# Kernel optimization log

Measured on AMD Instinct MI355X. Metric: run time of the kernel, lower is better.

Reference implementation:

```python
import jax, jax.numpy as jnp
import numpy as np

N_NODES = 50000
N_EDGES = 800000
E_DIM = 128
N_LAYERS = 3
IN_DIM = 2
OUT_DIM = 1


def _lin_init(key, fan_in, fan_out, scale=None):
    # rough kaiming-tanh init, exact values don't matter for correctness testing
    s = scale if scale is not None else (5.0 / 3.0) / np.sqrt(fan_in)
    return jax.random.normal(key, (fan_in, fan_out), dtype=jnp.float32) * s


def setup_inputs() -> dict:
    key = jax.random.key(0)
    ks = jax.random.split(key, 16)
    node_feature = jax.random.normal(ks[0], (N_NODES, IN_DIM), dtype=jnp.float32)
    edge_index = jax.random.randint(ks[1], (2, N_EDGES), 0, N_NODES)
    batch = jnp.zeros((N_NODES,), dtype=jnp.int32)

    enc_W = _lin_init(ks[2], IN_DIM, E_DIM)
    enc_b = jnp.zeros((E_DIM,), dtype=jnp.float32)

    def stack(k, fan_in, fan_out):
        kk = jax.random.split(k, N_LAYERS)
        return jnp.stack([_lin_init(kk[i], fan_in, fan_out) for i in range(N_LAYERS)])

    gate_W = stack(ks[3], E_DIM, E_DIM)
    gate_b = jnp.zeros((N_LAYERS, E_DIM), dtype=jnp.float32)
    att_W = stack(ks[4], E_DIM, E_DIM)
    att_b = jnp.zeros((N_LAYERS, E_DIM), dtype=jnp.float32)
    msg_W = stack(ks[5], E_DIM, E_DIM)
    msg_b = jnp.zeros((N_LAYERS, E_DIM), dtype=jnp.float32)
    upd_W = stack(ks[6], 2 * E_DIM, E_DIM)
    upd_b = jnp.zeros((N_LAYERS, E_DIM), dtype=jnp.float32)

    dec1_W = _lin_init(ks[7], E_DIM, E_DIM // 2)
    dec1_b = jnp.zeros((E_DIM // 2,), dtype=jnp.float32)
    dec2_W = _lin_init(ks[8], E_DIM // 2, OUT_DIM, scale=1.0 / np.sqrt(E_DIM // 2))
    dec2_b = jnp.zeros((OUT_DIM,), dtype=jnp.float32)

    return dict(node_feature=node_feature, edge_index=edge_index, batch=batch,
                enc_W=enc_W, enc_b=enc_b,
                gate_W=gate_W, gate_b=gate_b, att_W=att_W, att_b=att_b,
                msg_W=msg_W, msg_b=msg_b, upd_W=upd_W, upd_b=upd_b,
                dec1_W=dec1_W, dec1_b=dec1_b, dec2_W=dec2_W, dec2_b=dec2_b)


def _segment_softmax(x, seg, num_segments):
    # PyG softmax over segments, numerically stable, per-channel
    m = jax.ops.segment_max(x, seg, num_segments=num_segments)
    m = jnp.where(jnp.isfinite(m), m, 0.0)
    e = jnp.exp(x - m[seg])
    s = jax.ops.segment_sum(e, seg, num_segments=num_segments)
    return e / (s[seg] + 1e-16)


def reference(node_feature, edge_index, batch,
              enc_W, enc_b, gate_W, gate_b, att_W, att_b,
              msg_W, msg_b, upd_W, upd_b,
              dec1_W, dec1_b, dec2_W, dec2_b):
    n = node_feature.shape[0]
    src, dst = edge_index[0], edge_index[1]  # j -> i (source_to_target)
    h = jnp.tanh(node_feature @ enc_W + enc_b)  # [N, E_DIM]
    for l in range(N_LAYERS):
        mj = jnp.tanh(h[src] @ msg_W[l] + msg_b[l])          # messages [Edges, E_DIM]
        gate = mj @ gate_W[l] + gate_b[l]                     # gate_nn (Linear only)
        alpha = _segment_softmax(gate, dst, n)                # softmax over incoming edges
        v = jnp.tanh(mj @ att_W[l] + att_b[l])                # attention_mlp
        aggr = jax.ops.segment_sum(alpha * v, dst, num_segments=n)
        h = jnp.tanh(jnp.concatenate([h, aggr], axis=1) @ upd_W[l] + upd_b[l])
    out = jnp.tanh(h @ dec1_W + dec1_b)
    out = out @ dec2_W + dec2_b
    return out
```

## Files before the change

### kernel.cpp

```cpp
#include <hip/hip_runtime.h>
#include <math.h>

#define ED 128
#define PROW 256

typedef _Float16 f16;
typedef _Float16 half8 __attribute__((ext_vector_type(8)));
typedef _Float16 half4 __attribute__((ext_vector_type(4)));
typedef float f32x4 __attribute__((ext_vector_type(4)));

static __device__ __forceinline__ float tanh_fast(float x) {
  float ax = fabsf(x);
  float e = __expf(2.0f * ax);
  float t = 1.0f - 2.0f / (e + 1.0f);
  return __builtin_copysignf(t, x);
}

static __device__ __forceinline__ void stage_w(
    const char* __restrict__ gsrc, int rowBytes, int rowOff,
    char* lds, int tid, int nIter) {
  #pragma unroll
  for (int i = 0; i < nIter; ++i) {
    int b = (i * 256 + tid) * 16;
    int row = b >> 8;
    int sw = (b & 255) ^ ((row & 7) << 4);
    float4 v = *reinterpret_cast<const float4*>(
        gsrc + (size_t)row * rowBytes + rowOff + sw);
    *reinterpret_cast<float4*>(lds + b) = v;
  }
}

static __device__ __forceinline__ half8 read_w(const char* Wsb, int col, int koff) {
  int byte = col * 256 + (koff ^ ((col & 7) << 4));
  return *reinterpret_cast<const half8*>(Wsb + byte);
}

__global__ __launch_bounds__(256) void encoder_kernel(
    const float* __restrict__ x, const float* __restrict__ W,
    const float* __restrict__ b, f16* __restrict__ h, int n) {
  int idx = blockIdx.x * blockDim.x + threadIdx.x;
  if (idx >= n * ED) return;
  int i = idx >> 7, c = idx & 127;
  float v = x[i * 2 + 0] * W[c] + x[i * 2 + 1] * W[ED + c] + b[c];
  h[idx] = (f16)tanh_fast(v);
}

__global__ __launch_bounds__(256) void transpose_w_kernel(
    const float* __restrict__ src, f16* __restrict__ dst, int K, int C, int total) {
  int idx = blockIdx.x * 256 + threadIdx.x;
  if (idx >= total) return;
  int kc = K * C;
  int m = idx / kc;
  int rem = idx - m * kc;
  int c = rem / K;
  int k = rem - c * K;
  dst[idx] = (f16)src[(size_t)m * kc + (size_t)k * C + c];
}

__global__ __launch_bounds__(256) void transpose3_kernel(
    const float* __restrict__ s0, const float* __restrict__ s1,
    const float* __restrict__ s2, f16* __restrict__ d0,
    f16* __restrict__ d1, f16* __restrict__ d2) {
  int idx = blockIdx.x * 256 + threadIdx.x;
  const int per = 3 * 128 * 128;
  int which = idx / per;
  if (which >= 3) return;
  int rem = idx - which * per;
  const float* s = (which == 0) ? s0 : (which == 1) ? s1 : s2;
  f16* d = (which == 0) ? d0 : (which == 1) ? d1 : d2;
  int m = rem >> 14;
  int r2 = rem & 16383;
  int c = r2 >> 7, k = r2 & 127;
  d[rem] = (f16)s[m * 16384 + k * 128 + c];
}

__global__ __launch_bounds__(256) void count_deg_kernel(
    const int* __restrict__ dst, int* __restrict__ deg, int E) {
  int e = blockIdx.x * blockDim.x + threadIdx.x;
  if (e < E) atomicAdd(&deg[dst[e]], 1);
}

__global__ __launch_bounds__(1024) void scan_kernel(
    const int* __restrict__ deg, int* __restrict__ offs,
    int* __restrict__ cursor, int n) {
  __shared__ int wsum[16];
  __shared__ int carry_s;
  const int tid = threadIdx.x;
  const int lane = tid & 63;
  const int wid = tid >> 6;
  if (tid == 0) carry_s = 0;
  __syncthreads();
  for (int base = 0; base < n; base += 1024) {
    const int i = base + tid;
    const int v = (i < n) ? deg[i] : 0;
    int x = v;
    #pragma unroll
    for (int d = 1; d < 64; d <<= 1) {
      int t = __shfl_up(x, d, 64);
      if (lane >= d) x += t;
    }
    if (lane == 63) wsum[wid] = x;
    __syncthreads();
    int wbase = 0, total = 0;
    #pragma unroll
    for (int w = 0; w < 16; ++w) {
      int s = wsum[w];
      if (w < wid) wbase += s;
      total += s;
    }
    const int carry = carry_s;
    if (i < n) {
      const int excl = carry + wbase + x - v;
      offs[i] = excl;
      cursor[i] = excl;
    }
    __syncthreads();
    if (tid == 0) carry_s = carry + total;
    __syncthreads();
  }
  if (tid == 0) offs[n] = carry_s;
}

__global__ __launch_bounds__(256) void scatter_kernel(
    const int* __restrict__ src, const int* __restrict__ dst,
    int* __restrict__ cursor, int* __restrict__ ssrc, int E) {
  int e = blockIdx.x * blockDim.x + threadIdx.x;
  if (e < E) {
    int d = dst[e];
    int pos = atomicAdd(&cursor[d], 1);
    ssrc[pos] = src[e];
  }
}


__global__ __launch_bounds__(256) void gemm_mgv_kernel(
    const f16* __restrict__ h,
    const f16* __restrict__ mWt, const float* __restrict__ mb,
    const f16* __restrict__ gWt, const float* __restrict__ gb,
    const f16* __restrict__ aWt, const float* __restrict__ ab,
    f16* __restrict__ P, int n) {
  __shared__ f16 Ws[128 * 128];
  __shared__ f16 Ss[64 * 128];
  char* Wsb = reinterpret_cast<char*>(Ws);
  char* Sb = reinterpret_cast<char*>(Ss);
  const int tid = threadIdx.x;
  const int w = tid >> 6, lane = tid & 63;
  const int lr = lane & 15, lg = lane >> 4;
  const int r0 = blockIdx.x * 64 + w * 16;

  half8 a[4];
  {
    int rr = r0 + lr;
    if (rr >= n) rr = n - 1;
    const f16* ap = h + (size_t)rr * ED + lg * 8;
    #pragma unroll
    for (int kt = 0; kt < 4; ++kt)
      a[kt] = *reinterpret_cast<const half8*>(ap + kt * 32);
  }

  stage_w((const char*)mWt, 256, 0, Wsb, tid, 8);
  __syncthreads();
  #pragma unroll
  for (int t = 0; t < 8; ++t) {
    f32x4 acc = {0.f, 0.f, 0.f, 0.f};
    int col = t * 16 + lr;
    #pragma unroll
    for (int kt = 0; kt < 4; ++kt)
      acc = __builtin_amdgcn_mfma_f32_16x16x32_f16(a[kt], read_w(Wsb, col, lg * 16 + kt * 64), acc, 0, 0, 0);
    float bias = mb[col];
    #pragma unroll
    for (int j = 0; j < 4; ++j) {
      int srow = w * 16 + lg * 4 + j;
      int byte = srow * 256 + (((col * 2) ^ ((srow & 7) << 4)));
      *reinterpret_cast<f16*>(Sb + byte) = (f16)tanh_fast(acc[j] + bias);
    }
  }
  half8 ma[4];
  {
    int lrow = w * 16 + lr;
    #pragma unroll
    for (int kt = 0; kt < 4; ++kt) {
      int byte = lrow * 256 + ((lg * 16 + kt * 64) ^ ((lrow & 7) << 4));
      ma[kt] = *reinterpret_cast<const half8*>(Sb + byte);
    }
  }
  __syncthreads();

  stage_w((const char*)gWt, 256, 0, Wsb, tid, 8);
  __syncthreads();
  float wreg[8][4];
  #pragma unroll
  for (int t = 0; t < 8; ++t) {
    f32x4 acc = {0.f, 0.f, 0.f, 0.f};
    int col = t * 16 + lr;
    #pragma unroll
    for (int kt = 0; kt < 4; ++kt)
      acc = __builtin_amdgcn_mfma_f32_16x16x32_f16(ma[kt], read_w(Wsb, col, lg * 16 + kt * 64), acc, 0, 0, 0);
    float bias = gb[col];
    #pragma unroll
    for (int j = 0; j < 4; ++j) {
      float ww = fminf(__expf(acc[j] + bias), 60000.f);
      wreg[t][j] = ww;
      int grow = r0 + lg * 4 + j;
      if (grow < n) P[(size_t)grow * PROW + col] = (f16)ww;
    }
  }
  __syncthreads();

  stage_w((const char*)aWt, 256, 0, Wsb, tid, 8);
  __syncthreads();
  #pragma unroll
  for (int t = 0; t < 8; ++t) {
    f32x4 acc = {0.f, 0.f, 0.f, 0.f};
    int col = t * 16 + lr;
    #pragma unroll
    for (int kt = 0; kt < 4; ++kt)
      acc = __builtin_amdgcn_mfma_f32_16x16x32_f16(ma[kt], read_w(Wsb, col, lg * 16 + kt * 64), acc, 0, 0, 0);
    float bias = ab[col];
    #pragma unroll
    for (int j = 0; j < 4; ++j) {
      int grow = r0 + lg * 4 + j;
      if (grow < n)
        P[(size_t)grow * PROW + 128 + col] = (f16)(wreg[t][j] * tanh_fast(acc[j] + bias));
    }
  }
}

__global__ __launch_bounds__(256) void updmgv_kernel(
    const f16* __restrict__ h, const f16* __restrict__ ag,
    const f16* __restrict__ uWt, const float* __restrict__ ub,
    const f16* __restrict__ mWt, const float* __restrict__ mb,
    const f16* __restrict__ gWt, const float* __restrict__ gb,
    const f16* __restrict__ aWt, const float* __restrict__ ab,
    f16* __restrict__ hout, f16* __restrict__ P, int n) {
  __shared__ f16 Ws[128 * 128];
  __shared__ f16 Ss[64 * 128];
  char* Wsb = reinterpret_cast<char*>(Ws);
  char* Sb = reinterpret_cast<char*>(Ss);
  const int tid = threadIdx.x;
  const int w = tid >> 6, lane = tid & 63;
  const int lr = lane & 15, lg = lane >> 4;
  const int r0 = blockIdx.x * 64 + w * 16;

  half8 ah[4], aa[4];
  {
    int rr = r0 + lr;
    if (rr >= n) rr = n - 1;
    const f16* ap = h + (size_t)rr * ED + lg * 8;
    const f16* bp = ag + (size_t)rr * ED + lg * 8;
    #pragma unroll
    for (int kt = 0; kt < 4; ++kt) {
      ah[kt] = *reinterpret_cast<const half8*>(ap + kt * 32);
      aa[kt] = *reinterpret_cast<const half8*>(bp + kt * 32);
    }
  }

  stage_w((const char*)uWt, 512, 0, Wsb, tid, 8);
  __syncthreads();
  f32x4 acc8[8];
  #pragma unroll
  for (int t = 0; t < 8; ++t) {
    f32x4 acc = {0.f, 0.f, 0.f, 0.f};
    int col = t * 16 + lr;
    #pragma unroll
    for (int kt = 0; kt < 4; ++kt)
      acc = __builtin_amdgcn_mfma_f32_16x16x32_f16(ah[kt], read_w(Wsb, col, lg * 16 + kt * 64), acc, 0, 0, 0);
    acc8[t] = acc;
  }
  __syncthreads();
  stage_w((const char*)uWt, 512, 256, Wsb, tid, 8);
  __syncthreads();
  #pragma unroll
  for (int t = 0; t < 8; ++t) {
    f32x4 acc = acc8[t];
    int col = t * 16 + lr;
    #pragma unroll
    for (int kt = 0; kt < 4; ++kt)
      acc = __builtin_amdgcn_mfma_f32_16x16x32_f16(aa[kt], read_w(Wsb, col, lg * 16 + kt * 64), acc, 0, 0, 0);
    float bias = ub[col];
    #pragma unroll
    for (int j = 0; j < 4; ++j) {
      f16 hv = (f16)tanh_fast(acc[j] + bias);
      int srow = w * 16 + lg * 4 + j;
      int byte = srow * 256 + (((col * 2) ^ ((srow & 7) << 4)));
      *reinterpret_cast<f16*>(Sb + byte) = hv;
      int grow = r0 + lg * 4 + j;
      if (grow < n) hout[(size_t)grow * ED + col] = hv;
    }
  }
  half8 ha[4];
  {
    int lrow = w * 16 + lr;
    #pragma unroll
    for (int kt = 0; kt < 4; ++kt) {
      int byte = lrow * 256 + ((lg * 16 + kt * 64) ^ ((lrow & 7) << 4));
      ha[kt] = *reinterpret_cast<const half8*>(Sb + byte);
    }
  }
  __syncthreads();

  stage_w((const char*)mWt, 256, 0, Wsb, tid, 8);
  __syncthreads();
  #pragma unroll
  for (int t = 0; t < 8; ++t) {
    f32x4 acc = {0.f, 0.f, 0.f, 0.f};
    int col = t * 16 + lr;
    #pragma unroll
    for (int kt = 0; kt < 4; ++kt)
      acc = __builtin_amdgcn_mfma_f32_16x16x32_f16(ha[kt], read_w(Wsb, col, lg * 16 + kt * 64), acc, 0, 0, 0);
    float bias = mb[col];
    #pragma unroll
    for (int j = 0; j < 4; ++j) {
      int srow = w * 16 + lg * 4 + j;
      int byte = srow * 256 + (((col * 2) ^ ((srow & 7) << 4)));
      *reinterpret_cast<f16*>(Sb + byte) = (f16)tanh_fast(acc[j] + bias);
    }
  }
  half8 ma[4];
  {
    int lrow = w * 16 + lr;
    #pragma unroll
    for (int kt = 0; kt < 4; ++kt) {
      int byte = lrow * 256 + ((lg * 16 + kt * 64) ^ ((lrow & 7) << 4));
      ma[kt] = *reinterpret_cast<const half8*>(Sb + byte);
    }
  }
  __syncthreads();

  stage_w((const char*)gWt, 256, 0, Wsb, tid, 8);
  __syncthreads();
  float wreg[8][4];
  #pragma unroll
  for (int t = 0; t < 8; ++t) {
    f32x4 acc = {0.f, 0.f, 0.f, 0.f};
    int col = t * 16 + lr;
    #pragma unroll
    for (int kt = 0; kt < 4; ++kt)
      acc = __builtin_amdgcn_mfma_f32_16x16x32_f16(ma[kt], read_w(Wsb, col, lg * 16 + kt * 64), acc, 0, 0, 0);
    float bias = gb[col];
    #pragma unroll
    for (int j = 0; j < 4; ++j) {
      float ww = fminf(__expf(acc[j] + bias), 60000.f);
      wreg[t][j] = ww;
      int grow = r0 + lg * 4 + j;
      if (grow < n) P[(size_t)grow * PROW + col] = (f16)ww;
    }
  }
  __syncthreads();

  stage_w((const char*)aWt, 256, 0, Wsb, tid, 8);
  __syncthreads();
  #pragma unroll
  for (int t = 0; t < 8; ++t) {
    f32x4 acc = {0.f, 0.f, 0.f, 0.f};
    int col = t * 16 + lr;
    #pragma unroll
    for (int kt = 0; kt < 4; ++kt)
      acc = __builtin_amdgcn_mfma_f32_16x16x32_f16(ma[kt], read_w(Wsb, col, lg * 16 + kt * 64), acc, 0, 0, 0);
    float bias = ab[col];
    #pragma unroll
    for (int j = 0; j < 4; ++j) {
      int grow = r0 + lg * 4 + j;
      if (grow < n)
        P[(size_t)grow * PROW + 128 + col] = (f16)(wreg[t][j] * tanh_fast(acc[j] + bias));
    }
  }
}

__global__ __launch_bounds__(256) void upddec_kernel(
    const f16* __restrict__ h, const f16* __restrict__ ag,
    const f16* __restrict__ uWt, const float* __restrict__ ub,
    const f16* __restrict__ d1Wt, const float* __restrict__ d1b,
    const float* __restrict__ d2W, const float* __restrict__ d2b,
    float* __restrict__ out, int n) {
  __shared__ f16 Ws[128 * 128];
  __shared__ f16 Ss[64 * 128];
  char* Wsb = reinterpret_cast<char*>(Ws);
  char* Sb = reinterpret_cast<char*>(Ss);
  const int tid = threadIdx.x;
  const int w = tid >> 6, lane = tid & 63;
  const int lr = lane & 15, lg = lane >> 4;
  const int r0 = blockIdx.x * 64 + w * 16;

  half8 ah[4], aa[4];
  {
    int rr = r0 + lr;
    if (rr >= n) rr = n - 1;
    const f16* ap = h + (size_t)rr * ED + lg * 8;
    const f16* bp = ag + (size_t)rr * ED + lg * 8;
    #pragma unroll
    for (int kt = 0; kt < 4; ++kt) {
      ah[kt] = *reinterpret_cast<const half8*>(ap + kt * 32);
      aa[kt] = *reinterpret_cast<const half8*>(bp + kt * 32);
    }
  }

  stage_w((const char*)uWt, 512, 0, Wsb, tid, 8);
  __syncthreads();
  f32x4 acc8[8];
  #pragma unroll
  for (int t = 0; t < 8; ++t) {
    f32x4 acc = {0.f, 0.f, 0.f, 0.f};
    int col = t * 16 + lr;
    #pragma unroll
    for (int kt = 0; kt < 4; ++kt)
      acc = __builtin_amdgcn_mfma_f32_16x16x32_f16(ah[kt], read_w(Wsb, col, lg * 16 + kt * 64), acc, 0, 0, 0);
    acc8[t] = acc;
  }
  __syncthreads();
  stage_w((const char*)uWt, 512, 256, Wsb, tid, 8);
  __syncthreads();
  #pragma unroll
  for (int t = 0; t < 8; ++t) {
    f32x4 acc = acc8[t];
    int col = t * 16 + lr;
    #pragma unroll
    for (int kt = 0; kt < 4; ++kt)
      acc = __builtin_amdgcn_mfma_f32_16x16x32_f16(aa[kt], read_w(Wsb, col, lg * 16 + kt * 64), acc, 0, 0, 0);
    float bias = ub[col];
    #pragma unroll
    for (int j = 0; j < 4; ++j) {
      int srow = w * 16 + lg * 4 + j;
      int byte = srow * 256 + (((col * 2) ^ ((srow & 7) << 4)));
      *reinterpret_cast<f16*>(Sb + byte) = (f16)tanh_fast(acc[j] + bias);
    }
  }
  half8 ha[4];
  {
    int lrow = w * 16 + lr;
    #pragma unroll
    for (int kt = 0; kt < 4; ++kt) {
      int byte = lrow * 256 + ((lg * 16 + kt * 64) ^ ((lrow & 7) << 4));
      ha[kt] = *reinterpret_cast<const half8*>(Sb + byte);
    }
  }
  __syncthreads();

  stage_w((const char*)d1Wt, 256, 0, Wsb, tid, 4);
  __syncthreads();
  float rowsum[4] = {0.f, 0.f, 0.f, 0.f};
  #pragma unroll
  for (int t = 0; t < 4; ++t) {
    f32x4 acc = {0.f, 0.f, 0.f, 0.f};
    int col = t * 16 + lr;
    #pragma unroll
    for (int kt = 0; kt < 4; ++kt)
      acc = __builtin_amdgcn_mfma_f32_16x16x32_f16(ha[kt], read_w(Wsb, col, lg * 16 + kt * 64), acc, 0, 0, 0);
    float b1 = d1b[col], w2 = d2W[col];
    #pragma unroll
    for (int j = 0; j < 4; ++j) rowsum[j] += tanh_fast(acc[j] + b1) * w2;
  }
  #pragma unroll
  for (int d = 1; d < 16; d <<= 1) {
    #pragma unroll
    for (int j = 0; j < 4; ++j) rowsum[j] += __shfl_xor(rowsum[j], d, 64);
  }
  if (lr == 0) {
    #pragma unroll
    for (int j = 0; j < 4; ++j) {
      int grow = r0 + lg * 4 + j;
      if (grow < n) out[grow] = rowsum[j] + d2b[0];
    }
  }
}

__global__ __launch_bounds__(256) void edge_aggr_kernel(
    const int* __restrict__ offs, const int* __restrict__ ssrc,
    const f16* __restrict__ P, f16* __restrict__ aggr, int n) {
  int i = blockIdx.x * 4 + (threadIdx.x >> 6);
  if (i >= n) return;
  int lane = threadIdx.x & 63;
  int s0 = offs[i], s1 = offs[i + 1];
  const char* Pb = reinterpret_cast<const char*>(P);

  float4 acc = {0.f, 0.f, 0.f, 0.f};
  #pragma unroll 4
  for (int e = s0; e < s1; ++e) {
    int sn = ssrc[e];
    half4 x = *reinterpret_cast<const half4*>(Pb + (size_t)sn * 512 + lane * 8);
    acc.x += (float)x.x;
    acc.y += (float)x.y;
    acc.z += (float)x.z;
    acc.w += (float)x.w;
  }
  float px = __shfl(acc.x, lane ^ 32, 64);
  float py = __shfl(acc.y, lane ^ 32, 64);
  float pz = __shfl(acc.z, lane ^ 32, 64);
  float pw = __shfl(acc.w, lane ^ 32, 64);
  if (lane >= 32) {
    half4 o;
    o.x = (f16)(acc.x / (px + 1e-16f));
    o.y = (f16)(acc.y / (py + 1e-16f));
    o.z = (f16)(acc.z / (pz + 1e-16f));
    o.w = (f16)(acc.w / (pw + 1e-16f));
    *reinterpret_cast<half4*>(
        reinterpret_cast<char*>(aggr) + (size_t)i * 256 + (size_t)(lane - 32) * 8) = o;
  }
}

extern "C" void kernel_launch(void* const* d_in, const int* in_sizes, int n_in,
                              void* d_out, int out_size, void* d_ws, size_t ws_size,
                              hipStream_t stream) {
  const float* node_feature = (const float*)d_in[0];
  const int*   edge_index   = (const int*)d_in[1];
  const float* enc_W  = (const float*)d_in[3];
  const float* enc_b  = (const float*)d_in[4];
  const float* gate_W = (const float*)d_in[5];
  const float* gate_b = (const float*)d_in[6];
  const float* att_W  = (const float*)d_in[7];
  const float* att_b  = (const float*)d_in[8];
  const float* msg_W  = (const float*)d_in[9];
  const float* msg_b  = (const float*)d_in[10];
  const float* upd_W  = (const float*)d_in[11];
  const float* upd_b  = (const float*)d_in[12];
  const float* dec1_W = (const float*)d_in[13];
  const float* dec1_b = (const float*)d_in[14];
  const float* dec2_W = (const float*)d_in[15];
  const float* dec2_b = (const float*)d_in[16];

  const int n = in_sizes[0] / 2;
  const int E = in_sizes[1] / 2;
  const int* src = edge_index;
  const int* dst = edge_index + E;

  char* ws = (char*)d_ws;
  size_t off = 0;
  auto alloc = [&](size_t bytes) -> void* {
    void* p = ws + off;
    off += (bytes + 255) & ~(size_t)255;
    return p;
  };
  f16* hA   = (f16*)alloc((size_t)n * ED * 2);
  f16* hB   = (f16*)alloc((size_t)n * ED * 2);
  f16* P    = (f16*)alloc((size_t)n * PROW * 2);
  f16* aggr = (f16*)alloc((size_t)n * ED * 2);
  int* deg    = (int*)alloc((size_t)n * 4);
  int* offs   = (int*)alloc((size_t)(n + 1) * 4);
  int* cursor = (int*)alloc((size_t)n * 4);
  int* ssrc   = (int*)alloc((size_t)E * 4);
  f16* msgT  = (f16*)alloc((size_t)3 * ED * ED * 2);
  f16* gateT = (f16*)alloc((size_t)3 * ED * ED * 2);
  f16* attT  = (f16*)alloc((size_t)3 * ED * ED * 2);
  f16* updT  = (f16*)alloc((size_t)3 * ED * 2 * ED * 2);
  f16* dec1T = (f16*)alloc((size_t)ED * 64 * 2);

  {
    int tot3 = 3 * 3 * ED * ED;
    transpose3_kernel<<<(tot3 + 255) / 256, 256, 0, stream>>>(
        msg_W, gate_W, att_W, msgT, gateT, attT);
    int totu = 3 * 2 * ED * ED;
    transpose_w_kernel<<<(totu + 255) / 256, 256, 0, stream>>>(
        upd_W, updT, 2 * ED, ED, totu);
    int totd = ED * 64;
    transpose_w_kernel<<<(totd + 255) / 256, 256, 0, stream>>>(
        dec1_W, dec1T, ED, 64, totd);
  }

  hipMemsetAsync(deg, 0, (size_t)n * 4, stream);
  count_deg_kernel<<<(E + 255) / 256, 256, 0, stream>>>(dst, deg, E);
  scan_kernel<<<1, 1024, 0, stream>>>(deg, offs, cursor, n);
  scatter_kernel<<<(E + 255) / 256, 256, 0, stream>>>(src, dst, cursor, ssrc, E);

  encoder_kernel<<<((size_t)n * ED + 255) / 256, 256, 0, stream>>>(
      node_feature, enc_W, enc_b, hA, n);

  const int gemm_grid = (n + 63) / 64;
  const int aggr_grid = (n + 3) / 4;

  gemm_mgv_kernel<<<gemm_grid, 256, 0, stream>>>(
      hA, msgT, msg_b, gateT, gate_b, attT, att_b, P, n);
  edge_aggr_kernel<<<aggr_grid, 256, 0, stream>>>(offs, ssrc, P, aggr, n);

  updmgv_kernel<<<gemm_grid, 256, 0, stream>>>(
      hA, aggr, updT, upd_b,
      msgT + (size_t)1 * ED * ED, msg_b + ED,
      gateT + (size_t)1 * ED * ED, gate_b + ED,
      attT + (size_t)1 * ED * ED, att_b + ED,
      hB, P, n);
  edge_aggr_kernel<<<aggr_grid, 256, 0, stream>>>(offs, ssrc, P, aggr, n);

  updmgv_kernel<<<gemm_grid, 256, 0, stream>>>(
      hB, aggr, updT + (size_t)1 * 2 * ED * ED, upd_b + ED,
      msgT + (size_t)2 * ED * ED, msg_b + 2 * ED,
      gateT + (size_t)2 * ED * ED, gate_b + 2 * ED,
      attT + (size_t)2 * ED * ED, att_b + 2 * ED,
      hA, P, n);
  edge_aggr_kernel<<<aggr_grid, 256, 0, stream>>>(offs, ssrc, P, aggr, n);

  upddec_kernel<<<gemm_grid, 256, 0, stream>>>(
      hA, aggr, updT + (size_t)2 * 2 * ED * ED, upd_b + 2 * ED,
      dec1T, dec1_b, dec2_W, dec2_b, (float*)d_out, n);
}
```

Measured before the change: 467.1 us.

## Double GEMM block rows to 128 with 512 threads and restage update weights

The node GEMM kernels now run 512 threads over 128 rows per block, so each staged weight tile in LDS is reused by twice as many rows. The update GEMM stages both K halves at once for 64 output columns at a time, which removes the 8-register accumulator array. The gate weights are no longer held in registers across phases; they are re-read from the P buffer in global memory. Launch bounds ask for 4 blocks per CU to push occupancy, which adds global reads and tightens the register and LDS budget.

```diff
diff --git a/kernel.cpp b/kernel.cpp
--- a/kernel.cpp
+++ b/kernel.cpp
@@ -16,22 +16,39 @@
   return __builtin_copysignf(t, x);
 }
 
-static __device__ __forceinline__ void stage_w(
-    const char* __restrict__ gsrc, int rowBytes, int rowOff,
-    char* lds, int tid, int nIter) {
-  #pragma unroll
-  for (int i = 0; i < nIter; ++i) {
-    int b = (i * 256 + tid) * 16;
+template <int NT, int NBYTES>
+static __device__ __forceinline__ void stage256(
+    const char* __restrict__ gsrc, char* lds, int tid) {
+  #pragma unroll
+  for (int i = 0; i < NBYTES / (NT * 16); ++i) {
+    int b = (i * NT + tid) * 16;
     int row = b >> 8;
     int sw = (b & 255) ^ ((row & 7) << 4);
-    float4 v = *reinterpret_cast<const float4*>(
-        gsrc + (size_t)row * rowBytes + rowOff + sw);
+    float4 v = *reinterpret_cast<const float4*>(gsrc + (size_t)row * 256 + sw);
     *reinterpret_cast<float4*>(lds + b) = v;
   }
 }
 
 static __device__ __forceinline__ half8 read_w(const char* Wsb, int col, int koff) {
   int byte = col * 256 + (koff ^ ((col & 7) << 4));
+  return *reinterpret_cast<const half8*>(Wsb + byte);
+}
+
+template <int NT>
+static __device__ __forceinline__ void stage512(
+    const char* __restrict__ gsrc, char* lds, int tid) {
+  #pragma unroll
+  for (int i = 0; i < 32768 / (NT * 16); ++i) {
+    int b = (i * NT + tid) * 16;
+    int row = b >> 9;
+    int sw = (b & 511) ^ ((row & 7) << 4);
+    float4 v = *reinterpret_cast<const float4*>(gsrc + (size_t)row * 512 + sw);
+    *reinterpret_cast<float4*>(lds + b) = v;
+  }
+}
+
+static __device__ __forceinline__ half8 read_w512(const char* Wsb, int colL, int koff) {
+  int byte = colL * 512 + (koff ^ ((colL & 7) << 4));
   return *reinterpret_cast<const half8*>(Wsb + byte);
 }
 
@@ -133,20 +150,20 @@
 }
 
 
-__global__ __launch_bounds__(256) void gemm_mgv_kernel(
+__global__ __launch_bounds__(512, 4) void gemm_mgv_kernel(
     const f16* __restrict__ h,
     const f16* __restrict__ mWt, const float* __restrict__ mb,
     const f16* __restrict__ gWt, const float* __restrict__ gb,
     const f16* __restrict__ aWt, const float* __restrict__ ab,
     f16* __restrict__ P, int n) {
   __shared__ f16 Ws[128 * 128];
-  __shared__ f16 Ss[64 * 128];
+  __shared__ f16 Ss[128 * 128];
   char* Wsb = reinterpret_cast<char*>(Ws);
   char* Sb = reinterpret_cast<char*>(Ss);
   const int tid = threadIdx.x;
   const int w = tid >> 6, lane = tid & 63;
   const int lr = lane & 15, lg = lane >> 4;
-  const int r0 = blockIdx.x * 64 + w * 16;
+  const int r0 = blockIdx.x * 128 + w * 16;
 
   half8 a[4];
   {
@@ -158,7 +175,7 @@
       a[kt] = *reinterpret_cast<const half8*>(ap + kt * 32);
   }
 
-  stage_w((const char*)mWt, 256, 0, Wsb, tid, 8);
+  stage256<512, 32768>((const char*)mWt, Wsb, tid);
   __syncthreads();
   #pragma unroll
   for (int t = 0; t < 8; ++t) {
@@ -186,9 +203,8 @@
   }
   __syncthreads();
 
-  stage_w((const char*)gWt, 256, 0, Wsb, tid, 8);
-  __syncthreads();
-  float wreg[8][4];
+  stage256<512, 32768>((const char*)gWt, Wsb, tid);
+  __syncthreads();
   #pragma unroll
   for (int t = 0; t < 8; ++t) {
     f32x4 acc = {0.f, 0.f, 0.f, 0.f};
@@ -199,15 +215,14 @@
     float bias = gb[col];
     #pragma unroll
     for (int j = 0; j < 4; ++j) {
-      float ww = fminf(__expf(acc[j] + bias), 60000.f);
-      wreg[t][j] = ww;
       int grow = r0 + lg * 4 + j;
-      if (grow < n) P[(size_t)grow * PROW + col] = (f16)ww;
-    }
-  }
-  __syncthreads();
-
-  stage_w((const char*)aWt, 256, 0, Wsb, tid, 8);
+      if (grow < n)
+        P[(size_t)grow * PROW + col] = (f16)fminf(__expf(acc[j] + bias), 60000.f);
+    }
+  }
+  __syncthreads();
+
+  stage256<512, 32768>((const char*)aWt, Wsb, tid);
   __syncthreads();
   #pragma unroll
   for (int t = 0; t < 8; ++t) {
@@ -220,13 +235,15 @@
     #pragma unroll
     for (int j = 0; j < 4; ++j) {
       int grow = r0 + lg * 4 + j;
-      if (grow < n)
-        P[(size_t)grow * PROW + 128 + col] = (f16)(wreg[t][j] * tanh_fast(acc[j] + bias));
-    }
-  }
-}
-
-__global__ __launch_bounds__(256) void updmgv_kernel(
+      if (grow < n) {
+        float wld = (float)P[(size_t)grow * PROW + col];
+        P[(size_t)grow * PROW + 128 + col] = (f16)(wld * tanh_fast(acc[j] + bias));
+      }
+    }
+  }
+}
+
+__global__ __launch_bounds__(512, 4) void updmgv_kernel(
     const f16* __restrict__ h, const f16* __restrict__ ag,
     const f16* __restrict__ uWt, const float* __restrict__ ub,
     const f16* __restrict__ mWt, const float* __restrict__ mb,
@@ -234,13 +251,13 @@
     const f16* __restrict__ aWt, const float* __restrict__ ab,
     f16* __restrict__ hout, f16* __restrict__ P, int n) {
   __shared__ f16 Ws[128 * 128];
-  __shared__ f16 Ss[64 * 128];
+  __shared__ f16 Ss[128 * 128];
   char* Wsb = reinterpret_cast<char*>(Ws);
   char* Sb = reinterpret_cast<char*>(Ss);
   const int tid = threadIdx.x;
   const int w = tid >> 6, lane = tid & 63;
   const int lr = lane & 15, lg = lane >> 4;
-  const int r0 = blockIdx.x * 64 + w * 16;
+  const int r0 = blockIdx.x * 128 + w * 16;
 
   half8 ah[4], aa[4];
   {
@@ -255,37 +272,32 @@
     }
   }
 
-  stage_w((const char*)uWt, 512, 0, Wsb, tid, 8);
-  __syncthreads();
-  f32x4 acc8[8];
-  #pragma unroll
-  for (int t = 0; t < 8; ++t) {
-    f32x4 acc = {0.f, 0.f, 0.f, 0.f};
-    int col = t * 16 + lr;
-    #pragma unroll
-    for (int kt = 0; kt < 4; ++kt)
-      acc = __builtin_amdgcn_mfma_f32_16x16x32_f16(ah[kt], read_w(Wsb, col, lg * 16 + kt * 64), acc, 0, 0, 0);
-    acc8[t] = acc;
-  }
-  __syncthreads();
-  stage_w((const char*)uWt, 512, 256, Wsb, tid, 8);
-  __syncthreads();
-  #pragma unroll
-  for (int t = 0; t < 8; ++t) {
-    f32x4 acc = acc8[t];
-    int col = t * 16 + lr;
-    #pragma unroll
-    for (int kt = 0; kt < 4; ++kt)
-      acc = __builtin_amdgcn_mfma_f32_16x16x32_f16(aa[kt], read_w(Wsb, col, lg * 16 + kt * 64), acc, 0, 0, 0);
-    float bias = ub[col];
-    #pragma unroll
-    for (int j = 0; j < 4; ++j) {
-      f16 hv = (f16)tanh_fast(acc[j] + bias);
-      int srow = w * 16 + lg * 4 + j;
-      int byte = srow * 256 + (((col * 2) ^ ((srow & 7) << 4)));
-      *reinterpret_cast<f16*>(Sb + byte) = hv;
-      int grow = r0 + lg * 4 + j;
-      if (grow < n) hout[(size_t)grow * ED + col] = hv;
+  #pragma unroll
+  for (int half = 0; half < 2; ++half) {
+    __syncthreads();
+    stage512<512>((const char*)uWt + (size_t)half * 64 * 512, Wsb, tid);
+    __syncthreads();
+    #pragma unroll
+    for (int t = 0; t < 4; ++t) {
+      int colL = t * 16 + lr;
+      int col = half * 64 + colL;
+      f32x4 acc = {0.f, 0.f, 0.f, 0.f};
+      #pragma unroll
+      for (int kt = 0; kt < 4; ++kt)
+        acc = __builtin_amdgcn_mfma_f32_16x16x32_f16(ah[kt], read_w512(Wsb, colL, lg * 16 + kt * 64), acc, 0, 0, 0);
+      #pragma unroll
+      for (int kt = 0; kt < 4; ++kt)
+        acc = __builtin_amdgcn_mfma_f32_16x16x32_f16(aa[kt], read_w512(Wsb, colL, 256 + lg * 16 + kt * 64), acc, 0, 0, 0);
+      float bias = ub[col];
+      #pragma unroll
+      for (int j = 0; j < 4; ++j) {
+        f16 hv = (f16)tanh_fast(acc[j] + bias);
+        int srow = w * 16 + lg * 4 + j;
+        int byte = srow * 256 + (((col * 2) ^ ((srow & 7) << 4)));
+        *reinterpret_cast<f16*>(Sb + byte) = hv;
+        int grow = r0 + lg * 4 + j;
+        if (grow < n) hout[(size_t)grow * ED + col] = hv;
+      }
     }
   }
   half8 ha[4];
@@ -299,7 +311,7 @@
   }
   __syncthreads();
 
-  stage_w((const char*)mWt, 256, 0, Wsb, tid, 8);
+  stage256<512, 32768>((const char*)mWt, Wsb, tid);
   __syncthreads();
   #pragma unroll
   for (int t = 0; t < 8; ++t) {
@@ -327,9 +339,8 @@
   }
   __syncthreads();
 
-  stage_w((const char*)gWt, 256, 0, Wsb, tid, 8);
-  __syncthreads();
-  float wreg[8][4];
+  stage256<512, 32768>((const char*)gWt, Wsb, tid);
+  __syncthreads();
   #pragma unroll
   for (int t = 0; t < 8; ++t) {
     f32x4 acc = {0.f, 0.f, 0.f, 0.f};
@@ -340,15 +351,14 @@
     float bias = gb[col];
     #pragma unroll
     for (int j = 0; j < 4; ++j) {
-      float ww = fminf(__expf(acc[j] + bias), 60000.f);
-      wreg[t][j] = ww;
       int grow = r0 + lg * 4 + j;
-      if (grow < n) P[(size_t)grow * PROW + col] = (f16)ww;
-    }
-  }
-  __syncthreads();
-
-  stage_w((const char*)aWt, 256, 0, Wsb, tid, 8);
+      if (grow < n)
+        P[(size_t)grow * PROW + col] = (f16)fminf(__expf(acc[j] + bias), 60000.f);
+    }
+  }
+  __syncthreads();
+
+  stage256<512, 32768>((const char*)aWt, Wsb, tid);
   __syncthreads();
   #pragma unroll
   for (int t = 0; t < 8; ++t) {
@@ -361,26 +371,28 @@
     #pragma unroll
     for (int j = 0; j < 4; ++j) {
       int grow = r0 + lg * 4 + j;
-      if (grow < n)
-        P[(size_t)grow * PROW + 128 + col] = (f16)(wreg[t][j] * tanh_fast(acc[j] + bias));
-    }
-  }
-}
-
-__global__ __launch_bounds__(256) void upddec_kernel(
+      if (grow < n) {
+        float wld = (float)P[(size_t)grow * PROW + col];
+        P[(size_t)grow * PROW + 128 + col] = (f16)(wld * tanh_fast(acc[j] + bias));
+      }
+    }
+  }
+}
+
+__global__ __launch_bounds__(512, 4) void upddec_kernel(
     const f16* __restrict__ h, const f16* __restrict__ ag,
     const f16* __restrict__ uWt, const float* __restrict__ ub,
     const f16* __restrict__ d1Wt, const float* __restrict__ d1b,
     const float* __restrict__ d2W, const float* __restrict__ d2b,
     float* __restrict__ out, int n) {
   __shared__ f16 Ws[128 * 128];
-  __shared__ f16 Ss[64 * 128];
+  __shared__ f16 Ss[128 * 128];
   char* Wsb = reinterpret_cast<char*>(Ws);
   char* Sb = reinterpret_cast<char*>(Ss);
   const int tid = threadIdx.x;
   const int w = tid >> 6, lane = tid & 63;
   const int lr = lane & 15, lg = lane >> 4;
-  const int r0 = blockIdx.x * 64 + w * 16;
+  const int r0 = blockIdx.x * 128 + w * 16;
 
   half8 ah[4], aa[4];
   {
@@ -395,34 +407,29 @@
     }
   }
 
-  stage_w((const char*)uWt, 512, 0, Wsb, tid, 8);
-  __syncthreads();
-  f32x4 acc8[8];
-  #pragma unroll
-  for (int t = 0; t < 8; ++t) {
-    f32x4 acc = {0.f, 0.f, 0.f, 0.f};
-    int col = t * 16 + lr;
-    #pragma unroll
-    for (int kt = 0; kt < 4; ++kt)
-      acc = __builtin_amdgcn_mfma_f32_16x16x32_f16(ah[kt], read_w(Wsb, col, lg * 16 + kt * 64), acc, 0, 0, 0);
-    acc8[t] = acc;
-  }
-  __syncthreads();
-  stage_w((const char*)uWt, 512, 256, Wsb, tid, 8);
-  __syncthreads();
-  #pragma unroll
-  for (int t = 0; t < 8; ++t) {
-    f32x4 acc = acc8[t];
-    int col = t * 16 + lr;
-    #pragma unroll
-    for (int kt = 0; kt < 4; ++kt)
-      acc = __builtin_amdgcn_mfma_f32_16x16x32_f16(aa[kt], read_w(Wsb, col, lg * 16 + kt * 64), acc, 0, 0, 0);
-    float bias = ub[col];
-    #pragma unroll
-    for (int j = 0; j < 4; ++j) {
-      int srow = w * 16 + lg * 4 + j;
-      int byte = srow * 256 + (((col * 2) ^ ((srow & 7) << 4)));
-      *reinterpret_cast<f16*>(Sb + byte) = (f16)tanh_fast(acc[j] + bias);
+  #pragma unroll
+  for (int half = 0; half < 2; ++half) {
+    __syncthreads();
+    stage512<512>((const char*)uWt + (size_t)half * 64 * 512, Wsb, tid);
+    __syncthreads();
+    #pragma unroll
+    for (int t = 0; t < 4; ++t) {
+      int colL = t * 16 + lr;
+      int col = half * 64 + colL;
+      f32x4 acc = {0.f, 0.f, 0.f, 0.f};
+      #pragma unroll
+      for (int kt = 0; kt < 4; ++kt)
+        acc = __builtin_amdgcn_mfma_f32_16x16x32_f16(ah[kt], read_w512(Wsb, colL, lg * 16 + kt * 64), acc, 0, 0, 0);
+      #pragma unroll
+      for (int kt = 0; kt < 4; ++kt)
+        acc = __builtin_amdgcn_mfma_f32_16x16x32_f16(aa[kt], read_w512(Wsb, colL, 256 + lg * 16 + kt * 64), acc, 0, 0, 0);
+      float bias = ub[col];
+      #pragma unroll
+      for (int j = 0; j < 4; ++j) {
+        int srow = w * 16 + lg * 4 + j;
+        int byte = srow * 256 + (((col * 2) ^ ((srow & 7) << 4)));
+        *reinterpret_cast<f16*>(Sb + byte) = (f16)tanh_fast(acc[j] + bias);
+      }
     }
   }
   half8 ha[4];
@@ -436,7 +443,7 @@
   }
   __syncthreads();
 
-  stage_w((const char*)d1Wt, 256, 0, Wsb, tid, 4);
+  stage256<512, 16384>((const char*)d1Wt, Wsb, tid);
   __syncthreads();
   float rowsum[4] = {0.f, 0.f, 0.f, 0.f};
   #pragma unroll
@@ -564,14 +571,14 @@
   encoder_kernel<<<((size_t)n * ED + 255) / 256, 256, 0, stream>>>(
       node_feature, enc_W, enc_b, hA, n);
 
-  const int gemm_grid = (n + 63) / 64;
+  const int gemm_grid = (n + 127) / 128;
   const int aggr_grid = (n + 3) / 4;
 
-  gemm_mgv_kernel<<<gemm_grid, 256, 0, stream>>>(
+  gemm_mgv_kernel<<<gemm_grid, 512, 0, stream>>>(
       hA, msgT, msg_b, gateT, gate_b, attT, att_b, P, n);
   edge_aggr_kernel<<<aggr_grid, 256, 0, stream>>>(offs, ssrc, P, aggr, n);
 
-  updmgv_kernel<<<gemm_grid, 256, 0, stream>>>(
+  updmgv_kernel<<<gemm_grid, 512, 0, stream>>>(
       hA, aggr, updT, upd_b,
       msgT + (size_t)1 * ED * ED, msg_b + ED,
       gateT + (size_t)1 * ED * ED, gate_b + ED,
@@ -579,7 +586,7 @@
       hB, P, n);
   edge_aggr_kernel<<<aggr_grid, 256, 0, stream>>>(offs, ssrc, P, aggr, n);
 
-  updmgv_kernel<<<gemm_grid, 256, 0, stream>>>(
+  updmgv_kernel<<<gemm_grid, 512, 0, stream>>>(
       hB, aggr, updT + (size_t)1 * 2 * ED * ED, upd_b + ED,
       msgT + (size_t)2 * ED * ED, msg_b + 2 * ED,
       gateT + (size_t)2 * ED * ED, gate_b + 2 * ED,
@@ -587,7 +594,7 @@
       hA, P, n);
   edge_aggr_kernel<<<aggr_grid, 256, 0, stream>>>(offs, ssrc, P, aggr, n);
 
-  upddec_kernel<<<gemm_grid, 256, 0, stream>>>(
+  upddec_kernel<<<gemm_grid, 512, 0, stream>>>(
       hA, aggr, updT + (size_t)2 * 2 * ED * ED, upd_b + 2 * ED,
       dec1T, dec1_b, dec2_W, dec2_b, (float*)d_out, n);
 }
```

Result: faster. 447.9 us (median of 2 runs) (-4.1%).
